# Performance work log

Measured on AMD Instinct MI355X. Metric: run time of the kernel, lower is better.

Reference implementation:

```python
import jax, jax.numpy as jnp
import numpy as np

N, D, H, L = 50000, 128, 4, 3
E = 800000
C = D // H            # head dim = 32
NEG_SLOPE = 0.2       # PyG GATv2Conv default negative_slope
LN_EPS = 1e-5         # nn.LayerNorm default eps


def setup_inputs() -> dict:
    key = jax.random.key(0)
    ks = jax.random.split(key, 8)
    s = 1.0 / np.sqrt(D).astype(np.float32)
    return {
        "fine_poi_x": jax.random.normal(ks[0], (N, D), jnp.float32),
        "edge_index": jax.random.randint(ks[1], (2, E), 0, N, dtype=jnp.int32),
        "Wl": jax.random.normal(ks[2], (L, D, D), jnp.float32) * s,
        "bl": jnp.zeros((L, D), jnp.float32),
        "Wr": jax.random.normal(ks[3], (L, D, D), jnp.float32) * s,
        "br": jnp.zeros((L, D), jnp.float32),
        "att": jax.random.normal(ks[4], (L, H, C), jnp.float32) * s,
        "bias": jnp.zeros((L, D), jnp.float32),
        "gamma": jnp.ones((L, D), jnp.float32),
        "beta": jnp.zeros((L, D), jnp.float32),
    }


def _gatv2_conv(x, src, dst, Wl, bl, Wr, br, att, bias):
    # x: [N, D]; src/dst: [E'] (self-loops already appended)
    xl = (x @ Wl + bl).reshape(N, H, C)   # source-side transform (lin_l)
    xr = (x @ Wr + br).reshape(N, H, C)   # target-side transform (lin_r)
    m = xl[src] + xr[dst]                 # [E', H, C] per-edge pre-activation
    m = jax.nn.leaky_relu(m, NEG_SLOPE)
    e = jnp.einsum("ehc,hc->eh", m, att)  # [E', H] attention logits
    # segment softmax over edges grouped by destination node
    emax = jax.ops.segment_max(e, dst, num_segments=N)      # [N, H]
    ee = jnp.exp(e - emax[dst])
    denom = jax.ops.segment_sum(ee, dst, num_segments=N)    # [N, H]
    alpha = ee / denom[dst]               # self-loops guarantee denom >= 1 term
    out = jax.ops.segment_sum(xl[src] * alpha[:, :, None], dst, num_segments=N)
    return out.reshape(N, D) + bias


def _layernorm(x, g, b):
    mu = jnp.mean(x, axis=-1, keepdims=True)
    var = jnp.var(x, axis=-1, keepdims=True)
    return (x - mu) * jax.lax.rsqrt(var + LN_EPS) * g + b


def reference(fine_poi_x, edge_index, Wl, bl, Wr, br, att, bias, gamma, beta):
    # PyG GATv2Conv add_self_loops=True: append i->i edges
    loops = jnp.arange(N, dtype=edge_index.dtype)
    src = jnp.concatenate([edge_index[0], loops])
    dst = jnp.concatenate([edge_index[1], loops])
    x = fine_poi_x
    for i in range(L):
        h = _gatv2_conv(x, src, dst, Wl[i], bl[i], Wr[i], br[i], att[i], bias[i])
        x = _layernorm(x + h, gamma[i], beta[i])
        if i != L - 1:
            x = jax.nn.relu(x)
    return x
```

## Files before the change

kernel.cpp:

```cpp
#include <hip/hip_runtime.h>

#define N_NODES 50000
#define N_EDGES 800000
#define DIM 128
#define TOT_EDGES (N_EDGES + N_NODES)
#define LOG2E 1.44269504088896f

#define BSHIFT 9
#define BNODES 512
#define NB ((N_NODES + BNODES - 1) / BNODES)
#define BCAP 16384
#define EPB 4096
#define EPT 16
#define NBLK_A ((TOT_EDGES + EPB - 1) / EPB)

typedef __attribute__((ext_vector_type(8))) _Float16 f16x8;
typedef __attribute__((ext_vector_type(2))) _Float16 h2;
typedef __attribute__((ext_vector_type(4))) float f32x4;
typedef decltype(__builtin_amdgcn_cvt_pkrtz(0.f, 0.f)) fp16v2;

__device__ inline uint h2u(h2 v) { return __builtin_bit_cast(uint, v); }
__device__ inline h2 u2h(uint v) { return __builtin_bit_cast(h2, v); }
__device__ inline uint pk2u(fp16v2 v) { return __builtin_bit_cast(uint, v); }

__device__ inline float rowsum16(float v) {
  int x;
  x = __builtin_amdgcn_update_dpp(0, __float_as_int(v), 0x128, 0xF, 0xF, true);
  v += __int_as_float(x);
  x = __builtin_amdgcn_update_dpp(0, __float_as_int(v), 0x124, 0xF, 0xF, true);
  v += __int_as_float(x);
  x = __builtin_amdgcn_update_dpp(0, __float_as_int(v), 0x122, 0xF, 0xF, true);
  v += __int_as_float(x);
  x = __builtin_amdgcn_update_dpp(0, __float_as_int(v), 0x121, 0xF, 0xF, true);
  v += __int_as_float(x);
  return v;
}


__global__ __launch_bounds__(256) void partA_kernel(const int* __restrict__ srcArr,
                                                    const int* __restrict__ dstArr,
                                                    int* __restrict__ bcnt,
                                                    uint2* __restrict__ bbuf) {
  int tid = threadIdx.x;
  int e0 = blockIdx.x * EPB;
  __shared__ int hist[NB], base[NB], loff[NB];
  if (tid < NB) { hist[tid] = 0; loff[tid] = 0; }
  __syncthreads();

  int sv[EPT], dv[EPT];
#pragma unroll
  for (int i = 0; i < EPT; ++i) {
    int e = e0 + i * 256 + tid;
    int s = 0, d = -1;
    if (e < TOT_EDGES) {
      if (e < N_EDGES) { s = srcArr[e]; d = dstArr[e]; }
      else { s = e - N_EDGES; d = s; }
    }
    sv[i] = s; dv[i] = d;
    if (d >= 0) atomicAdd(&hist[d >> BSHIFT], 1);
  }
  __syncthreads();
  if (tid < NB) {
    int h = hist[tid];
    if (h > 0) base[tid] = atomicAdd(&bcnt[tid], h);
  }
  __syncthreads();
#pragma unroll
  for (int i = 0; i < EPT; ++i) {
    int d = dv[i];
    if (d >= 0) {
      int b = d >> BSHIFT;
      int p = atomicAdd(&loff[b], 1);
      bbuf[(size_t)b * BCAP + base[b] + p] = make_uint2((uint)sv[i], (uint)d);
    }
  }
}

__global__ __launch_bounds__(128) void scanb_kernel(const int* __restrict__ bcnt,
                                                    int* __restrict__ colbase,
                                                    int* __restrict__ rowptr) {
  int tid = threadIdx.x;
  int v = (tid < NB) ? bcnt[tid] : 0;
  __shared__ int s[128];
  s[tid] = v;
  __syncthreads();
  for (int off = 1; off < 128; off <<= 1) {
    int t = (tid >= off) ? s[tid - off] : 0;
    __syncthreads();
    s[tid] += t;
    __syncthreads();
  }
  if (tid < NB) colbase[tid] = s[tid] - v;
  if (tid == 0) rowptr[N_NODES] = TOT_EDGES;
}


__global__ __launch_bounds__(512) void partB_kernel(const uint2* __restrict__ bbuf,
                                                    const int* __restrict__ bcnt,
                                                    const int* __restrict__ colbase,
                                                    int* __restrict__ rowptr,
                                                    int* __restrict__ col) {
  int b = blockIdx.x, tid = threadIdx.x;
  int m = bcnt[b];
  int cb = colbase[b];
  const uint2* buf = bbuf + (size_t)b * BCAP;

  __shared__ int cnt[BNODES], scn[BNODES], cur[BNODES];
  cnt[tid] = 0;
  __syncthreads();
  for (int e = tid; e < m; e += 512) {
    int d = (int)buf[e].y;
    atomicAdd(&cnt[d & (BNODES - 1)], 1);
  }
  __syncthreads();
  int c = cnt[tid];
  scn[tid] = c;
  __syncthreads();
  for (int off = 1; off < BNODES; off <<= 1) {
    int t = (tid >= off) ? scn[tid - off] : 0;
    __syncthreads();
    scn[tid] += t;
    __syncthreads();
  }
  int excl = scn[tid] - c;
  int node = b * BNODES + tid;
  if (node < N_NODES) rowptr[node] = cb + excl;
  cur[tid] = excl;
  __syncthreads();
  for (int e = tid; e < m; e += 512) {
    uint2 sd = buf[e];
    int p = atomicAdd(&cur[(int)sd.y & (BNODES - 1)], 1);
    col[cb + p] = (int)sd.x;
  }
}


__global__ __launch_bounds__(256) void convx_kernel(const float* __restrict__ x,
                                                    uint* __restrict__ xb) {
  int t = blockIdx.x * 256 + threadIdx.x;
  if (t < N_NODES * (DIM / 2)) {
    float2 v = ((const float2*)x)[t];
    xb[t] = pk2u(__builtin_amdgcn_cvt_pkrtz(v.x, v.y));
  }
}

__global__ __launch_bounds__(256) void convw_kernel(const float* __restrict__ Wl,
                                                    const float* __restrict__ Wr,
                                                    ushort* __restrict__ Wt) {
  int t = blockIdx.x * 256 + threadIdx.x;
  if (t >= 3 * 2 * DIM * DIM) return;
  int k = t & 127;
  int n = (t >> 7) & 127;
  int w = (t >> 14) & 1;
  int l = t >> 15;
  const float* W = w ? Wr : Wl;
  _Float16 h = (_Float16)W[l * DIM * DIM + k * DIM + n];
  Wt[t] = __builtin_bit_cast(ushort, h);
}

__global__ __launch_bounds__(192) void conva_kernel(const float* __restrict__ att,
                                                    uint* __restrict__ attc) {
  int t = threadIdx.x;
  float a0 = att[2 * t] * LOG2E, a1 = att[2 * t + 1] * LOG2E;
  attc[t] = pk2u(__builtin_amdgcn_cvt_pkrtz(a0, a1));
}


__global__ __launch_bounds__(256) void gemm_mfma_kernel(
    const uint* __restrict__ xb,
    const ushort* __restrict__ Wt,
    const float* __restrict__ bl, const float* __restrict__ br,
    uint* __restrict__ xl, uint* __restrict__ xr) {
  int wave = threadIdx.x >> 6, lane = threadIdx.x & 63;
  int lr = lane & 15, kq = lane >> 4;
  int m0 = blockIdx.x * 64;

  const ushort* W = Wt + (wave >> 1) * (DIM * DIM);
  const float* bias = (wave >> 1) ? br : bl;
  uint* outp = (wave >> 1) ? xr : xl;
  int n0 = (wave & 1) * 64;

  f16x8 bfrag[4][4];
#pragma unroll
  for (int nt = 0; nt < 4; ++nt)
#pragma unroll
    for (int kt = 0; kt < 4; ++kt)
      bfrag[nt][kt] = *(const f16x8*)(W + (n0 + nt * 16 + lr) * DIM + kt * 32 + kq * 8);

  f32x4 acc[4][4];
#pragma unroll
  for (int mt = 0; mt < 4; ++mt)
#pragma unroll
    for (int nt = 0; nt < 4; ++nt)
      acc[mt][nt] = (f32x4){0.f, 0.f, 0.f, 0.f};

#pragma unroll
  for (int mt = 0; mt < 4; ++mt) {
    int m = m0 + mt * 16 + lr;
    int mc = m < N_NODES ? m : N_NODES - 1;
    f16x8 afrag[4];
#pragma unroll
    for (int kt = 0; kt < 4; ++kt)
      afrag[kt] = *(const f16x8*)((const ushort*)xb + (size_t)mc * DIM + kt * 32 + kq * 8);
#pragma unroll
    for (int nt = 0; nt < 4; ++nt)
#pragma unroll
      for (int kt = 0; kt < 4; ++kt)
        acc[mt][nt] = __builtin_amdgcn_mfma_f32_16x16x32_f16(bfrag[nt][kt], afrag[kt],
                                                             acc[mt][nt], 0, 0, 0);
  }

#pragma unroll
  for (int mt = 0; mt < 4; ++mt) {
    int m = m0 + mt * 16 + lr;
    if (m < N_NODES) {
#pragma unroll
      for (int nt = 0; nt < 4; ++nt) {
        int n = n0 + nt * 16 + kq * 4;
        float4 bb = *(const float4*)(bias + n);
        uint2 o;
        o.x = pk2u(__builtin_amdgcn_cvt_pkrtz(acc[mt][nt][0] + bb.x, acc[mt][nt][1] + bb.y));
        o.y = pk2u(__builtin_amdgcn_cvt_pkrtz(acc[mt][nt][2] + bb.z, acc[mt][nt][3] + bb.w));
        *(uint2*)(outp + (size_t)m * (DIM / 2) + (n >> 1)) = o;
      }
    }
  }
}


__global__ __launch_bounds__(64) void att_kernel(
    const float* __restrict__ xin, const uint* __restrict__ xlb,
    const uint* __restrict__ xrb, const int* __restrict__ rowptr,
    const int* __restrict__ col, const uint* __restrict__ attc,
    const float* __restrict__ bias, const float* __restrict__ gamma,
    const float* __restrict__ beta, float* __restrict__ xoutf,
    uint* __restrict__ xoutb, int do_relu) {
  int lane = threadIdx.x;
  int n = blockIdx.x;
  size_t rowp = (size_t)n * (DIM / 2) + lane;

  h2 r2 = u2h(xrb[rowp]);
  h2 at2 = u2h(attc[lane]);
  const h2 c02 = {(_Float16)0.2f, (_Float16)0.2f};
  float acc0 = 0.f, acc1 = 0.f, den = 0.f;

  int js = rowptr[n], je = rowptr[n + 1];
  int jm = je - 1;

#define CIDX(j) col[(j) < jm ? (j) : jm]
#define GATHER(dst, cv, j)                                                  \
  {                                                                         \
    dst = 0u;                                                               \
    if ((j) < je)                                                           \
      dst = xlb[(size_t)__builtin_amdgcn_readfirstlane(cv) * (DIM / 2) + lane]; \
  }

  int c0 = CIDX(js), c1 = CIDX(js + 1), c2 = CIDX(js + 2), c3 = CIDX(js + 3);
  uint g0, g1, g2, g3;
  GATHER(g0, c0, js); GATHER(g1, c1, js + 1);
  GATHER(g2, c2, js + 2); GATHER(g3, c3, js + 3);
  int q0 = CIDX(js + 4), q1 = CIDX(js + 5), q2 = CIDX(js + 6), q3 = CIDX(js + 7);

  for (int base = js; base < je; base += 4) {
    uint h0, h1, h2v_, h3;
    GATHER(h0, q0, base + 4); GATHER(h1, q1, base + 5);
    GATHER(h2v_, q2, base + 6); GATHER(h3, q3, base + 7);
    int t0 = CIDX(base + 8), t1 = CIDX(base + 9);
    int t2 = CIDX(base + 10), t3 = CIDX(base + 11);

#define PROC(i, g)                                            \
  {                                                           \
    h2 a2 = u2h(g);                                           \
    h2 s2 = a2 + r2;                                          \
    h2 m2 = __builtin_elementwise_max(s2, s2 * c02);          \
    float p = __builtin_amdgcn_fdot2(                         \
        __builtin_bit_cast(fp16v2, m2),                       \
        __builtin_bit_cast(fp16v2, at2), 0.f, false);         \
    p = rowsum16(p);                                          \
    float w = (base + (i) < je) ? __builtin_amdgcn_exp2f(p) : 0.f; \
    den += w;                                                 \
    acc0 = fmaf(w, (float)a2.x, acc0);                        \
    acc1 = fmaf(w, (float)a2.y, acc1);                        \
  }
    PROC(0, g0); PROC(1, g1); PROC(2, g2); PROC(3, g3);
#undef PROC
    g0 = h0; g1 = h1; g2 = h2v_; g3 = h3;
    q0 = t0; q1 = t1; q2 = t2; q3 = t3;
  }
#undef CIDX
#undef GATHER

  float inv = 1.0f / den;
  float2 xi = ((const float2*)xin)[rowp];
  float2 bi = ((const float2*)bias)[lane];
  float o0 = fmaf(acc0, inv, bi.x + xi.x);
  float o1 = fmaf(acc1, inv, bi.y + xi.y);

  float s1 = o0 + o1, s2 = o0 * o0 + o1 * o1;
  s1 = rowsum16(s1);
  s2 = rowsum16(s2);
  s1 += __shfl_xor(s1, 16, 64);
  s2 += __shfl_xor(s2, 16, 64);
  s1 += __shfl_xor(s1, 32, 64);
  s2 += __shfl_xor(s2, 32, 64);
  float mean = s1 * (1.0f / DIM);
  float var = s2 * (1.0f / DIM) - mean * mean;
  float rstd = rsqrtf(var + 1e-5f);
  float2 gm = ((const float2*)gamma)[lane];
  float2 bt = ((const float2*)beta)[lane];
  float y0 = (o0 - mean) * rstd * gm.x + bt.x;
  float y1 = (o1 - mean) * rstd * gm.y + bt.y;
  if (do_relu) { y0 = fmaxf(y0, 0.f); y1 = fmaxf(y1, 0.f); }
  ((float2*)xoutf)[rowp] = make_float2(y0, y1);
  if (xoutb) xoutb[rowp] = pk2u(__builtin_amdgcn_cvt_pkrtz(y0, y1));
}


extern "C" void kernel_launch(void* const* d_in, const int* in_sizes, int n_in,
                              void* d_out, int out_size, void* d_ws, size_t ws_size,
                              hipStream_t stream) {
  const float* x_in  = (const float*)d_in[0];
  const int*   eidx  = (const int*)d_in[1];
  const float* Wl    = (const float*)d_in[2];
  const float* bl    = (const float*)d_in[3];
  const float* Wr    = (const float*)d_in[4];
  const float* br    = (const float*)d_in[5];
  const float* att   = (const float*)d_in[6];
  const float* bias  = (const float*)d_in[7];
  const float* gamma = (const float*)d_in[8];
  const float* beta  = (const float*)d_in[9];
  float* out = (float*)d_out;

  char* p = (char*)d_ws;
  auto alloc = [&](size_t bytes) {
    char* q = p;
    p += (bytes + 255) & ~(size_t)255;
    return q;
  };
  uint*  xb       = (uint*)alloc((size_t)N_NODES * (DIM / 2) * 4);
  uint*  xlb      = (uint*)alloc((size_t)N_NODES * (DIM / 2) * 4);
  uint*  xrb      = (uint*)alloc((size_t)N_NODES * (DIM / 2) * 4);
  float* xA       = (float*)alloc((size_t)N_NODES * DIM * 4);
  ushort* Wt      = (ushort*)alloc((size_t)3 * 2 * DIM * DIM * 2);
  uint*  attc     = (uint*)alloc((size_t)3 * 64 * 4);
  int*   rowptr   = (int*)alloc((size_t)(N_NODES + 1) * 4);
  int*   col      = (int*)alloc((size_t)TOT_EDGES * 4);
  uint2* bbuf     = (uint2*)alloc((size_t)NB * BCAP * 8);
  int*   bcnt     = (int*)alloc((size_t)NB * 4);
  int*   colbase  = (int*)alloc((size_t)NB * 4);

  (void)hipMemsetAsync(bcnt, 0, (size_t)NB * 4, stream);
  partA_kernel<<<NBLK_A, 256, 0, stream>>>(eidx, eidx + N_EDGES, bcnt, bbuf);
  scanb_kernel<<<1, 128, 0, stream>>>(bcnt, colbase, rowptr);
  partB_kernel<<<NB, 512, 0, stream>>>(bbuf, bcnt, colbase, rowptr, col);
  convx_kernel<<<(N_NODES * (DIM / 2) + 255) / 256, 256, 0, stream>>>(x_in, xb);
  convw_kernel<<<(3 * 2 * DIM * DIM + 255) / 256, 256, 0, stream>>>(Wl, Wr, Wt);
  conva_kernel<<<1, 192, 0, stream>>>(att, attc);

  const float* xcur_f = x_in;
  for (int l = 0; l < 3; ++l) {
    gemm_mfma_kernel<<<(N_NODES + 63) / 64, 256, 0, stream>>>(
        xb, Wt + (size_t)l * 2 * DIM * DIM, bl + l * DIM, br + l * DIM, xlb, xrb);
    float* xnext_f = (l == 2) ? out : xA;
    uint* xnext_b = (l == 2) ? nullptr : xb;
    att_kernel<<<N_NODES, 64, 0, stream>>>(
        xcur_f, xlb, xrb, rowptr, col, attc + l * 64, bias + l * DIM,
        gamma + l * DIM, beta + l * DIM, xnext_f, xnext_b, (l != 2) ? 1 : 0);
    xcur_f = xnext_f;
  }
}
```

Baseline: 266.0 us.

## Batch-load edge indices per wavefront and carry residual in fp16 buffer

The attention kernel now loads up to 64 column indices at once with one coalesced per-lane load and broadcasts each with readlane. This replaces the per-edge index loads that sat in the gather loop. The residual input is now read from the fp16 activation buffer and written back in place, so the fp32 intermediate activation buffer and its writes in non-final layers are gone. The trade-off is that the residual path loses precision, since it now rounds through fp16 every layer.

```diff
diff --git a/kernel.cpp b/kernel.cpp
--- a/kernel.cpp
+++ b/kernel.cpp
@@ -93,7 +93,6 @@
   if (tid < NB) colbase[tid] = s[tid] - v;
   if (tid == 0) rowptr[N_NODES] = TOT_EDGES;
 }
-
 
 __global__ __launch_bounds__(512) void partB_kernel(const uint2* __restrict__ bbuf,
                                                     const int* __restrict__ bcnt,
@@ -229,12 +228,12 @@
 
 
 __global__ __launch_bounds__(64) void att_kernel(
-    const float* __restrict__ xin, const uint* __restrict__ xlb,
+    const uint* __restrict__ xinb, const uint* __restrict__ xlb,
     const uint* __restrict__ xrb, const int* __restrict__ rowptr,
     const int* __restrict__ col, const uint* __restrict__ attc,
     const float* __restrict__ bias, const float* __restrict__ gamma,
-    const float* __restrict__ beta, float* __restrict__ xoutf,
-    uint* __restrict__ xoutb, int do_relu) {
+    const float* __restrict__ beta, uint* __restrict__ xoutb,
+    float* __restrict__ xoutf, int do_relu) {
   int lane = threadIdx.x;
   int n = blockIdx.x;
   size_t rowp = (size_t)n * (DIM / 2) + lane;
@@ -247,54 +246,56 @@
   int js = rowptr[n], je = rowptr[n + 1];
   int jm = je - 1;
 
-#define CIDX(j) col[(j) < jm ? (j) : jm]
-#define GATHER(dst, cv, j)                                                  \
-  {                                                                         \
-    dst = 0u;                                                               \
-    if ((j) < je)                                                           \
-      dst = xlb[(size_t)__builtin_amdgcn_readfirstlane(cv) * (DIM / 2) + lane]; \
-  }
-
-  int c0 = CIDX(js), c1 = CIDX(js + 1), c2 = CIDX(js + 2), c3 = CIDX(js + 3);
-  uint g0, g1, g2, g3;
-  GATHER(g0, c0, js); GATHER(g1, c1, js + 1);
-  GATHER(g2, c2, js + 2); GATHER(g3, c3, js + 3);
-  int q0 = CIDX(js + 4), q1 = CIDX(js + 5), q2 = CIDX(js + 6), q3 = CIDX(js + 7);
-
-  for (int base = js; base < je; base += 4) {
-    uint h0, h1, h2v_, h3;
-    GATHER(h0, q0, base + 4); GATHER(h1, q1, base + 5);
-    GATHER(h2v_, q2, base + 6); GATHER(h3, q3, base + 7);
-    int t0 = CIDX(base + 8), t1 = CIDX(base + 9);
-    int t2 = CIDX(base + 10), t3 = CIDX(base + 11);
-
-#define PROC(i, g)                                            \
-  {                                                           \
-    h2 a2 = u2h(g);                                           \
-    h2 s2 = a2 + r2;                                          \
-    h2 m2 = __builtin_elementwise_max(s2, s2 * c02);          \
-    float p = __builtin_amdgcn_fdot2(                         \
-        __builtin_bit_cast(fp16v2, m2),                       \
-        __builtin_bit_cast(fp16v2, at2), 0.f, false);         \
-    p = rowsum16(p);                                          \
-    float w = (base + (i) < je) ? __builtin_amdgcn_exp2f(p) : 0.f; \
-    den += w;                                                 \
-    acc0 = fmaf(w, (float)a2.x, acc0);                        \
-    acc1 = fmaf(w, (float)a2.y, acc1);                        \
-  }
-    PROC(0, g0); PROC(1, g1); PROC(2, g2); PROC(3, g3);
+  int ci = js + lane;
+  uint colv = (uint)col[ci < jm ? ci : jm];
+
+  for (int cbase = js; cbase < je; cbase += 64) {
+    int cnt = je - cbase;
+    if (cnt > 64) cnt = 64;
+    int cm = cnt - 1;
+    uint colv_next = colv;
+    if (cbase + 64 < je) {
+      int ci2 = cbase + 64 + lane;
+      colv_next = (uint)col[ci2 < jm ? ci2 : jm];
+    }
+
+#define GLD(dst, e)                                                          \
+  {                                                                          \
+    int s_ = __builtin_amdgcn_readlane((int)colv, (e) < cm ? (e) : cm);      \
+    dst = xlb[(size_t)s_ * (DIM / 2) + lane];                                \
+  }
+    uint g0, g1, g2, g3;
+    GLD(g0, 0) GLD(g1, 1) GLD(g2, 2) GLD(g3, 3)
+    for (int e = 0; e < cnt; e += 4) {
+      uint n0_, n1_, n2_, n3_;
+      GLD(n0_, e + 4) GLD(n1_, e + 5) GLD(n2_, e + 6) GLD(n3_, e + 7)
+#define PROC(i, g)                                                 \
+  {                                                                \
+    h2 a2 = u2h(g);                                                \
+    h2 s2 = a2 + r2;                                               \
+    h2 m2 = __builtin_elementwise_max(s2, s2 * c02);               \
+    float p = __builtin_amdgcn_fdot2(                              \
+        __builtin_bit_cast(fp16v2, m2),                            \
+        __builtin_bit_cast(fp16v2, at2), 0.f, false);              \
+    p = rowsum16(p);                                               \
+    float w = (e + (i) < cnt) ? __builtin_amdgcn_exp2f(p) : 0.f;   \
+    den += w;                                                      \
+    acc0 = fmaf(w, (float)a2.x, acc0);                             \
+    acc1 = fmaf(w, (float)a2.y, acc1);                             \
+  }
+      PROC(0, g0) PROC(1, g1) PROC(2, g2) PROC(3, g3)
 #undef PROC
-    g0 = h0; g1 = h1; g2 = h2v_; g3 = h3;
-    q0 = t0; q1 = t1; q2 = t2; q3 = t3;
-  }
-#undef CIDX
-#undef GATHER
+      g0 = n0_; g1 = n1_; g2 = n2_; g3 = n3_;
+    }
+#undef GLD
+    colv = colv_next;
+  }
 
   float inv = 1.0f / den;
-  float2 xi = ((const float2*)xin)[rowp];
+  h2 xi2 = u2h(xinb[rowp]);
   float2 bi = ((const float2*)bias)[lane];
-  float o0 = fmaf(acc0, inv, bi.x + xi.x);
-  float o1 = fmaf(acc1, inv, bi.y + xi.y);
+  float o0 = fmaf(acc0, inv, bi.x + (float)xi2.x);
+  float o1 = fmaf(acc1, inv, bi.y + (float)xi2.y);
 
   float s1 = o0 + o1, s2 = o0 * o0 + o1 * o1;
   s1 = rowsum16(s1);
@@ -311,8 +312,8 @@
   float y0 = (o0 - mean) * rstd * gm.x + bt.x;
   float y1 = (o1 - mean) * rstd * gm.y + bt.y;
   if (do_relu) { y0 = fmaxf(y0, 0.f); y1 = fmaxf(y1, 0.f); }
-  ((float2*)xoutf)[rowp] = make_float2(y0, y1);
   if (xoutb) xoutb[rowp] = pk2u(__builtin_amdgcn_cvt_pkrtz(y0, y1));
+  if (xoutf) ((float2*)xoutf)[rowp] = make_float2(y0, y1);
 }
 
 
@@ -340,7 +341,6 @@
   uint*  xb       = (uint*)alloc((size_t)N_NODES * (DIM / 2) * 4);
   uint*  xlb      = (uint*)alloc((size_t)N_NODES * (DIM / 2) * 4);
   uint*  xrb      = (uint*)alloc((size_t)N_NODES * (DIM / 2) * 4);
-  float* xA       = (float*)alloc((size_t)N_NODES * DIM * 4);
   ushort* Wt      = (ushort*)alloc((size_t)3 * 2 * DIM * DIM * 2);
   uint*  attc     = (uint*)alloc((size_t)3 * 64 * 4);
   int*   rowptr   = (int*)alloc((size_t)(N_NODES + 1) * 4);
@@ -357,15 +357,12 @@
   convw_kernel<<<(3 * 2 * DIM * DIM + 255) / 256, 256, 0, stream>>>(Wl, Wr, Wt);
   conva_kernel<<<1, 192, 0, stream>>>(att, attc);
 
-  const float* xcur_f = x_in;
   for (int l = 0; l < 3; ++l) {
     gemm_mfma_kernel<<<(N_NODES + 63) / 64, 256, 0, stream>>>(
         xb, Wt + (size_t)l * 2 * DIM * DIM, bl + l * DIM, br + l * DIM, xlb, xrb);
-    float* xnext_f = (l == 2) ? out : xA;
-    uint* xnext_b = (l == 2) ? nullptr : xb;
     att_kernel<<<N_NODES, 64, 0, stream>>>(
-        xcur_f, xlb, xrb, rowptr, col, attc + l * 64, bias + l * DIM,
-        gamma + l * DIM, beta + l * DIM, xnext_f, xnext_b, (l != 2) ? 1 : 0);
-    xcur_f = xnext_f;
-  }
-}
+        xb, xlb, xrb, rowptr, col, attc + l * 64, bias + l * DIM,
+        gamma + l * DIM, beta + l * DIM,
+        (l == 2) ? nullptr : xb, (l == 2) ? out : nullptr, (l != 2) ? 1 : 0);
+  }
+}
```

Result: faster. 252.1 us (-5.2%).
